# Performance work log

Measured on AMD Instinct MI355X. Metric: run time of the kernel, lower is better.

Reference implementation:

```python
import jax, jax.numpy as jnp
import numpy as np

HEAD_DIM = 128
N_HEADS = 32
DIM = 4096
SEQ = 2048
BSZ = 2


def apply_rotary(x, cos, sin):
    # x: [b, s, h, d]; cos/sin: [s, d//2]
    xr = x.reshape(*x.shape[:-1], -1, 2)  # [b, s, h, d/2, 2]
    xe, xo = xr[..., 0], xr[..., 1]
    c = cos[None, :, None, :]
    s = sin[None, :, None, :]
    oe = xe * c - xo * s
    oo = xe * s + xo * c
    return jnp.stack([oe, oo], axis=-1).reshape(x.shape)


def setup_inputs() -> dict:
    key = jax.random.key(0)
    ks = jax.random.split(key, 8)
    x = jax.random.normal(ks[0], (BSZ, SEQ, DIM), dtype=jnp.float32)
    scale = 1.0 / np.sqrt(DIM)
    wq = jax.random.normal(ks[1], (DIM, DIM), dtype=jnp.float32) * scale
    wk = jax.random.normal(ks[2], (DIM, DIM), dtype=jnp.float32) * scale
    wv = jax.random.normal(ks[3], (DIM, DIM), dtype=jnp.float32) * scale
    wo = jax.random.normal(ks[4], (DIM, DIM), dtype=jnp.float32) * scale
    # RoPE frequencies (LLaMA convention)
    inv_freq = 1.0 / (10000.0 ** (np.arange(0, HEAD_DIM, 2, dtype=np.float32) / HEAD_DIM))
    t = np.arange(SEQ, dtype=np.float32)
    angles = np.outer(t, inv_freq)  # [S, d/2]
    freqs_cos = jnp.asarray(np.cos(angles))
    freqs_sin = jnp.asarray(np.sin(angles))
    # additive causal mask
    mask = jnp.where(jnp.triu(jnp.ones((SEQ, SEQ), dtype=bool), k=1), -jnp.inf, 0.0)
    mask = mask.astype(jnp.float32)[None, None, :, :]
    return {"x": x, "wq": wq, "wk": wk, "wv": wv, "wo": wo,
            "freqs_cos": freqs_cos, "freqs_sin": freqs_sin, "mask": mask,
            "start_pos": 0}


def reference(x, wq, wk, wv, wo, freqs_cos, freqs_sin, mask, start_pos):
    bsz, seqlen, _ = x.shape
    xq = (x @ wq.T).reshape(bsz, seqlen, N_HEADS, HEAD_DIM)
    xk = (x @ wk.T).reshape(bsz, seqlen, N_HEADS, HEAD_DIM)
    xv = (x @ wv.T).reshape(bsz, seqlen, N_HEADS, HEAD_DIM)
    xq = apply_rotary(xq, freqs_cos, freqs_sin)
    xk = apply_rotary(xk, freqs_cos, freqs_sin)
    # [b, h, s, d]
    q = xq.transpose(0, 2, 1, 3)
    k = xk.transpose(0, 2, 1, 3)
    v = xv.transpose(0, 2, 1, 3)
    scores = jnp.einsum("bhqd,bhkd->bhqk", q, k) / np.sqrt(HEAD_DIM)
    scores = scores + mask
    probs = jax.nn.softmax(scores.astype(jnp.float32), axis=-1).astype(q.dtype)
    out = jnp.einsum("bhqk,bhkd->bhqd", probs, v)
    out = out.transpose(0, 2, 1, 3).reshape(bsz, seqlen, -1)
    return out @ wo.T
```

## Files before the change

### kernel.cpp

```cpp
#include <hip/hip_runtime.h>
#include <stdint.h>

#define DIMK 4096
#define HD 128
#define NH 32
#define SEQL 2048
#define BSZN 2
#define NROWS (BSZN*SEQL)

typedef __bf16 bf16x8 __attribute__((ext_vector_type(8)));
typedef float f32x4 __attribute__((ext_vector_type(4)));
typedef unsigned short u16;
typedef unsigned int u32;

__device__ __forceinline__ float bf2f(u16 h){
  u32 u = ((u32)h) << 16; float f;
  __builtin_memcpy(&f, &u, 4); return f;
}
__device__ __forceinline__ u16 f2bf(float f){
  u32 u; __builtin_memcpy(&u, &f, 4);
  return (u16)((u + 0x7fffu + ((u >> 16) & 1u)) >> 16);
}

__device__ __forceinline__ void gld_lds16(const void* g, void* l){
  __builtin_amdgcn_global_load_lds(
      (__attribute__((address_space(1))) void*)(uintptr_t)g,
      (__attribute__((address_space(3))) void*)(uintptr_t)l, 16, 0, 0);
}

#define BARX __builtin_amdgcn_s_barrier()
#define LGKM0 asm volatile("s_waitcnt lgkmcnt(0)" ::: "memory")
#define VMC6  asm volatile("s_waitcnt vmcnt(6)"  ::: "memory")
#define SP1 __builtin_amdgcn_s_setprio(1)
#define SP0 __builtin_amdgcn_s_setprio(0)

#define LDA4(MB, Ab) do{ \
  _Pragma("unroll") for (int mi = 0; mi < 4; ++mi){ \
    const int m_ = (MB) + mi; \
    const short* _p = (Ab) + (m_>>2)*8192 + (m_&3)*2048 + rdA; \
    aF[mi][0] = *(const bf16x8*)(_p + ch0); \
    aF[mi][1] = *(const bf16x8*)(_p + ch1); } }while(0)

#define LDB2(NB, Bb) do{ \
  _Pragma("unroll") for (int ni = 0; ni < 2; ++ni){ \
    const int n_ = (NB) + ni; \
    const short* _p = (Bb) + (n_>>1)*8192 + (n_&1)*4096 + rdB; \
    bF[ni][0] = *(const bf16x8*)(_p + ch0); \
    bF[ni][1] = *(const bf16x8*)(_p + ch1); } }while(0)

#define MFMA16(MB, NB) do{ \
  _Pragma("unroll") for (int ks = 0; ks < 2; ++ks) \
  _Pragma("unroll") for (int mi = 0; mi < 4; ++mi) \
  _Pragma("unroll") for (int ni = 0; ni < 2; ++ni) \
    acc[(MB)+mi][(NB)+ni] = __builtin_amdgcn_mfma_f32_16x16x32_bf16( \
        aF[mi][ks], bF[ni][ks], acc[(MB)+mi][(NB)+ni], 0, 0, 0); }while(0)

#define STG_A(buf,h,kt) do{ \
    size_t _o = ((size_t)(h)<<19) + (size_t)(kt)*64; \
    short* _d = dA + (buf)*32768 + (h)*8192; \
    gld_lds16(sA[0]+_o, _d); gld_lds16(sA[1]+_o, _d+512); }while(0)

#define STG_B(buf,h,kt) do{ \
    size_t _o = ((size_t)(h)<<19) + (size_t)(kt)*64; \
    short* _d = dB + (buf)*32768 + (h)*8192; \
    gld_lds16(sB[0]+_o, _d); gld_lds16(sB[1]+_o, _d+512); }while(0)

template<int OUTF32>
__device__ __forceinline__ void gemm256_core(const u16* __restrict__ A,
                                             const u16* __restrict__ B,
                                             void* __restrict__ Cv,
                                             short* SMEM)
{
  const int tid  = threadIdx.x;
  const int wave = tid >> 6, lane = tid & 63;
  const int wm = wave >> 2, wn = wave & 3;
  const int g = lane >> 4, c16 = lane & 15;

  const int bid = blockIdx.x;
  const int xcd = bid & 7, cc = bid >> 3;
  const int bx = (xcd & 3)*4 + (cc & 3);
  const int by = (xcd >> 2)*8 + (cc >> 2);
  const int m0 = bx*256, n0 = by*256;

  const int ch0 = ((g ^ (c16 & 7)) << 3);
  const int ch1 = ch0 ^ 32;
  const int rdA = wm*1024 + c16*64;
  const int rdB = wn*1024 + c16*64;

  const int swzc = (((lane & 7) ^ ((lane >> 3) & 7)) << 3);
  const u16* sA[2]; const u16* sB[2];
  #pragma unroll
  for (int p = 0; p < 2; ++p){
    int rr = wave*16 + p*8 + (lane >> 3);
    sA[p] = A + (size_t)(m0 + rr)*DIMK + swzc;
    sB[p] = B + (size_t)(n0 + rr)*DIMK + swzc;
  }
  short* const dA = SMEM + wave*1024;
  short* const dB = SMEM + 16384 + wave*1024;

  const short* A0 = SMEM;
  const short* B0 = SMEM + 16384;
  const short* A1 = SMEM + 32768;
  const short* B1 = SMEM + 49152;

  f32x4 acc[8][4];
  #pragma unroll
  for (int m = 0; m < 8; ++m)
    #pragma unroll
    for (int n = 0; n < 4; ++n)
      acc[m][n] = (f32x4){0.f, 0.f, 0.f, 0.f};

  bf16x8 aF[4][2], bF[2][2];

  STG_A(0,0,0); STG_B(0,1,0); STG_A(0,1,0); STG_B(0,0,0);
  STG_A(1,0,1); STG_B(1,1,1); STG_A(1,1,1);
  VMC6; BARX;

  #pragma unroll 1
  for (int i = 0; i < 32; ++i){
    const int t1 = (2*i+1) & 63, t2 = (2*i+2) & 63, t3 = (2*i+3) & 63;
    LDA4(0, A0); LDB2(0, B0);
    STG_B(1, 0, t1);
    BARX; LGKM0;
    SP1; MFMA16(0, 0); SP0;
    BARX;
    LDB2(2, B0);
    STG_A(0, 0, t2);
    BARX; LGKM0;
    SP1; MFMA16(0, 2); SP0;
    BARX;
    LDA4(4, A0);
    STG_B(0, 1, t2);
    BARX; LGKM0;
    SP1; MFMA16(4, 2); SP0;
    BARX;
    LDB2(0, B0);
    STG_A(0, 1, t2);
    VMC6;
    BARX; LGKM0;
    SP1; MFMA16(4, 0); SP0;
    BARX;
    LDA4(0, A1); LDB2(0, B1);
    STG_B(0, 0, t2);
    BARX; LGKM0;
    SP1; MFMA16(0, 0); SP0;
    BARX;
    LDB2(2, B1);
    STG_A(1, 0, t3);
    BARX; LGKM0;
    SP1; MFMA16(0, 2); SP0;
    BARX;
    LDA4(4, A1);
    STG_B(1, 1, t3);
    BARX; LGKM0;
    SP1; MFMA16(4, 2); SP0;
    BARX;
    LDB2(0, B1);
    STG_A(1, 1, t3);
    VMC6;
    BARX; LGKM0;
    SP1; MFMA16(4, 0); SP0;
    BARX;
  }

  if constexpr (OUTF32 == 0){
    u16* C = (u16*)Cv;
    #pragma unroll
    for (int m = 0; m < 8; ++m){
      int row0 = m0 + (m*2 + wm)*16 + g*4;
      #pragma unroll
      for (int n = 0; n < 4; ++n){
        int col = n0 + (n*4 + wn)*16 + c16;
        #pragma unroll
        for (int r = 0; r < 4; ++r)
          C[(size_t)(row0 + r)*DIMK + col] = f2bf(acc[m][n][r]);
      }
    }
  } else {
    float* C = (float*)Cv;
    #pragma unroll
    for (int m = 0; m < 8; ++m){
      int row0 = m0 + (m*2 + wm)*16 + g*4;
      #pragma unroll
      for (int n = 0; n < 4; ++n){
        int col = n0 + (n*4 + wn)*16 + c16;
        #pragma unroll
        for (int r = 0; r < 4; ++r)
          C[(size_t)(row0 + r)*DIMK + col] = acc[m][n][r];
      }
    }
  }
}

__global__ __launch_bounds__(512, 2) void gemm_bf16_kernel(const u16* __restrict__ A,
    const u16* __restrict__ B, u16* __restrict__ C)
{
  __shared__ __align__(16) short SMEM[65536];
  gemm256_core<0>(A, B, C, SMEM);
}

__global__ __launch_bounds__(512, 2) void gemm_f32_kernel(const u16* __restrict__ A,
    const u16* __restrict__ B, float* __restrict__ C)
{
  __shared__ __align__(16) short SMEM[65536];
  gemm256_core<1>(A, B, C, SMEM);
}

__global__ __launch_bounds__(256) void cvt_kernel(const float* __restrict__ src,
                                                  u16* __restrict__ dst, int n8)
{
  int t = blockIdx.x*256 + threadIdx.x;
  if (t >= n8) return;
  const f32x4* s = (const f32x4*)src + (size_t)t*2;
  f32x4 a = s[0], b = s[1];
  ushort4 lo, hi;
  lo.x = f2bf(a[0]); lo.y = f2bf(a[1]); lo.z = f2bf(a[2]); lo.w = f2bf(a[3]);
  hi.x = f2bf(b[0]); hi.y = f2bf(b[1]); hi.z = f2bf(b[2]); hi.w = f2bf(b[3]);
  ushort4* d = (ushort4*)dst + (size_t)t*2;
  d[0] = lo; d[1] = hi;
}

__global__ __launch_bounds__(256) void transpose_kernel(const u16* __restrict__ v,
                                                        u16* __restrict__ vt)
{
  __shared__ u16 tile[64][72];
  const int t  = threadIdx.x;
  const int s0 = blockIdx.x * 64;
  const int d0 = blockIdx.y * 64;
  const int bh = blockIdx.z;
  const int b = bh >> 5, h = bh & 31;

  #pragma unroll
  for (int i = 0; i < 4; ++i){
    int row = i*16 + (t >> 4);
    int cc  = (t & 15) * 4;
    uint2 val = *(const uint2*)(v + (size_t)(b*SEQL + s0 + row)*DIMK + h*HD + d0 + cc);
    const u16* p4 = (const u16*)&val;
    #pragma unroll
    for (int j = 0; j < 4; ++j) tile[cc + j][row] = p4[j];
  }
  __syncthreads();
  #pragma unroll
  for (int i = 0; i < 4; ++i){
    int drow = i*16 + (t >> 4);
    int sc   = (t & 15) * 4;
    uint2 o; u16* po = (u16*)&o;
    #pragma unroll
    for (int j = 0; j < 4; ++j) po[j] = tile[drow][sc + j];
    *(uint2*)(vt + ((size_t)(b*NH + h)*HD + d0 + drow)*SEQL + s0 + sc) = o;
  }
}

__global__ __launch_bounds__(256) void rope_kernel(const u16* __restrict__ qsrc,
    const u16* __restrict__ ksrc, u16* __restrict__ qdst, u16* __restrict__ kdst,
    const float* __restrict__ fc, const float* __restrict__ fs)
{
  const size_t PER = (size_t)NROWS * DIMK / 8;
  size_t t = (size_t)blockIdx.x * 256 + threadIdx.x;
  const u16* src = qsrc; u16* dst = qdst;
  if (t >= PER){ src = ksrc; dst = kdst; t -= PER; }
  size_t e0 = t * 8;
  int row = (int)(e0 >> 12);
  int col = (int)(e0 & (DIMK-1));
  int s  = row & (SEQL-1);
  int i0 = (col & (HD-1)) >> 1;

  uint4 raw = *(const uint4*)(src + e0);
  u16* xs = (u16*)&raw;
  f32x4 c4 = *(const f32x4*)(fc + s*64 + i0);
  f32x4 s4 = *(const f32x4*)(fs + s*64 + i0);
  #pragma unroll
  for (int j = 0; j < 4; ++j){
    float e = bf2f(xs[2*j]), o = bf2f(xs[2*j+1]);
    float c = c4[j], sn = s4[j];
    xs[2*j]   = f2bf(e*c - o*sn);
    xs[2*j+1] = f2bf(e*sn + o*c);
  }
  *(uint4*)(dst + e0) = raw;
}

__device__ __forceinline__ void stage_k_tile(const u16* kb, int s0, short* Ksd,
                                             int wave, int g, int c16){
  #pragma unroll
  for (int it = 0; it < 4; ++it){
    int rbase = it*16 + wave*4;
    int row = rbase + g;
    gld_lds16(kb + (size_t)(s0 + row)*DIMK + ((c16 ^ (row & 7)) << 3),
              Ksd + rbase*128);
  }
}
__device__ __forceinline__ void stage_v_tile(const u16* vb, int s0, short* Vd,
                                             int wave, int lane){
  const int sc = lane & 7, rg = lane >> 3;
  #pragma unroll
  for (int it = 0; it < 4; ++it){
    int rbase = (it*4 + wave)*8;
    int row = rbase + rg;
    gld_lds16(vb + (size_t)row*SEQL + s0 + ((sc ^ (row & 7)) << 3),
              Vd + rbase*64);
  }
}

__global__ __launch_bounds__(256) void flash_kernel(const u16* __restrict__ Q,
    const u16* __restrict__ K, const u16* __restrict__ Vt, u16* __restrict__ AO)
{
  __shared__ short Ks[64*128];
  __shared__ short Vs[2*128*64];
  __shared__ short Ps[4*32*64];

  const int bh = blockIdx.x;
  const int qt = 15 - (int)blockIdx.y;
  const int b = bh >> 5, h = bh & 31;
  const int tid = threadIdx.x;
  const int wave = tid >> 6, lane = tid & 63;
  const int g = lane >> 4, c16 = lane & 15;
  const int qr0 = qt*128 + wave*32;

  const u16* kb = K  + (size_t)(b*SEQL)*DIMK + h*HD;
  const u16* vb = Vt + (size_t)(b*NH + h)*HD*SEQL;
  short* Pw = Ps + wave*(32*64);

  stage_k_tile(kb, 0, Ks, wave, g, c16);
  stage_v_tile(vb, 0, Vs, wave, lane);

  bf16x8 qa[2][4];
  #pragma unroll
  for (int rt = 0; rt < 2; ++rt){
    const u16* qp = Q + (size_t)(b*SEQL + qr0 + rt*16 + c16)*DIMK + h*HD + g*8;
    #pragma unroll
    for (int kc = 0; kc < 4; ++kc)
      qa[rt][kc] = *(const bf16x8*)(qp + kc*32);
  }

  f32x4 oacc[2][8];
  #pragma unroll
  for (int rt = 0; rt < 2; ++rt)
    #pragma unroll
    for (int dt = 0; dt < 8; ++dt)
      oacc[rt][dt] = (f32x4){0.f, 0.f, 0.f, 0.f};
  float m_st[2][4], l_st[2][4];
  #pragma unroll
  for (int rt = 0; rt < 2; ++rt)
    #pragma unroll
    for (int r = 0; r < 4; ++r){ m_st[rt][r] = -1e30f; l_st[rt][r] = 0.f; }

  const int nsteps = 2*(qt + 1);
  for (int kt = 0; kt < nsteps; ++kt){
    const int s0 = kt*64;
    const short* Vsc = Vs + (kt & 1)*(128*64);
    const bool alive = (s0 <= qr0 + 31);

    __syncthreads();

    f32x4 sacc[2][4];
    if (alive){
      #pragma unroll
      for (int rt = 0; rt < 2; ++rt)
        #pragma unroll
        for (int ct = 0; ct < 4; ++ct)
          sacc[rt][ct] = (f32x4){0.f, 0.f, 0.f, 0.f};
      __builtin_amdgcn_s_setprio(1);
      #pragma unroll
      for (int kc = 0; kc < 4; ++kc){
        #pragma unroll
        for (int ct = 0; ct < 4; ++ct){
          int row = ct*16 + c16;
          bf16x8 bfr = *(const bf16x8*)(Ks + row*128 + (((g + 4*kc) ^ (row & 7)) << 3));
          sacc[0][ct] = __builtin_amdgcn_mfma_f32_16x16x32_bf16(qa[0][kc], bfr, sacc[0][ct], 0, 0, 0);
          sacc[1][ct] = __builtin_amdgcn_mfma_f32_16x16x32_bf16(qa[1][kc], bfr, sacc[1][ct], 0, 0, 0);
        }
      }
      __builtin_amdgcn_s_setprio(0);
    }

    __syncthreads();

    if (kt + 1 < nsteps){
      stage_k_tile(kb, s0 + 64, Ks, wave, g, c16);
      stage_v_tile(vb, s0 + 64, Vs + ((kt+1) & 1)*(128*64), wave, lane);
    }

    if (alive){
      const float scale = 0.08838834764831845f;
      #pragma unroll
      for (int rt = 0; rt < 2; ++rt){
        int rowb = qr0 + rt*16 + g*4;
        #pragma unroll
        for (int ct = 0; ct < 4; ++ct){
          int scol = s0 + ct*16 + c16;
          #pragma unroll
          for (int r = 0; r < 4; ++r){
            float v = sacc[rt][ct][r] * scale;
            sacc[rt][ct][r] = (scol <= rowb + r) ? v : -1e30f;
          }
        }
      }

      #pragma unroll
      for (int rt = 0; rt < 2; ++rt){
        #pragma unroll
        for (int r = 0; r < 4; ++r){
          float mx = fmaxf(fmaxf(sacc[rt][0][r], sacc[rt][1][r]),
                           fmaxf(sacc[rt][2][r], sacc[rt][3][r]));
          #pragma unroll
          for (int off = 1; off < 16; off <<= 1)
            mx = fmaxf(mx, __shfl_xor(mx, off));
          float mn = fmaxf(m_st[rt][r], mx);
          float al = __expf(m_st[rt][r] - mn);
          m_st[rt][r] = mn;
          float sum = 0.f;
          #pragma unroll
          for (int ct = 0; ct < 4; ++ct){
            float pv = __expf(sacc[rt][ct][r] - mn);
            sacc[rt][ct][r] = pv;
            sum += pv;
          }
          #pragma unroll
          for (int off = 1; off < 16; off <<= 1)
            sum += __shfl_xor(sum, off);
          l_st[rt][r] = l_st[rt][r]*al + sum;
          #pragma unroll
          for (int dt = 0; dt < 8; ++dt)
            oacc[rt][dt][r] *= al;
        }
      }

      #pragma unroll
      for (int rt = 0; rt < 2; ++rt)
        #pragma unroll
        for (int ct = 0; ct < 4; ++ct)
          #pragma unroll
          for (int r = 0; r < 4; ++r){
            int prow = rt*16 + g*4 + r;
            int pcol = ct*16 + c16;
            Pw[prow*64 + ((((pcol >> 3) ^ (prow & 7)) << 3) | (pcol & 7))] =
                (short)f2bf(sacc[rt][ct][r]);
          }

      asm volatile("s_waitcnt lgkmcnt(0)" ::: "memory");
      __builtin_amdgcn_sched_barrier(0);

      __builtin_amdgcn_s_setprio(1);
      #pragma unroll
      for (int kc2 = 0; kc2 < 2; ++kc2){
        int pr0 = c16, pr1 = 16 + c16;
        bf16x8 pf0 = *(const bf16x8*)(Pw + pr0*64 + (((g + 4*kc2) ^ (pr0 & 7)) << 3));
        bf16x8 pf1 = *(const bf16x8*)(Pw + pr1*64 + (((g + 4*kc2) ^ (pr1 & 7)) << 3));
        #pragma unroll
        for (int dt = 0; dt < 8; ++dt){
          int vr = dt*16 + c16;
          bf16x8 vf = *(const bf16x8*)(Vsc + vr*64 + (((g + 4*kc2) ^ (vr & 7)) << 3));
          oacc[0][dt] = __builtin_amdgcn_mfma_f32_16x16x32_bf16(pf0, vf, oacc[0][dt], 0, 0, 0);
          oacc[1][dt] = __builtin_amdgcn_mfma_f32_16x16x32_bf16(pf1, vf, oacc[1][dt], 0, 0, 0);
        }
      }
      __builtin_amdgcn_s_setprio(0);
    }
  }

  #pragma unroll
  for (int rt = 0; rt < 2; ++rt){
    float inv[4];
    #pragma unroll
    for (int r = 0; r < 4; ++r) inv[r] = 1.0f / l_st[rt][r];
    #pragma unroll
    for (int dt = 0; dt < 8; ++dt){
      #pragma unroll
      for (int r = 0; r < 4; ++r){
        int qrow = qr0 + rt*16 + g*4 + r;
        int col  = h*HD + dt*16 + c16;
        AO[(size_t)(b*SEQL + qrow)*DIMK + col] = f2bf(oacc[rt][dt][r] * inv[r]);
      }
    }
  }
}

extern "C" void kernel_launch(void* const* d_in, const int* in_sizes, int n_in,
                              void* d_out, int out_size, void* d_ws, size_t ws_size,
                              hipStream_t stream)
{
  const float* x  = (const float*)d_in[0];
  const float* wq = (const float*)d_in[1];
  const float* wk = (const float*)d_in[2];
  const float* wv = (const float*)d_in[3];
  const float* wo = (const float*)d_in[4];
  const float* fc = (const float*)d_in[5];
  const float* fs = (const float*)d_in[6];
  float* out = (float*)d_out;

  const size_t TEN  = (size_t)NROWS * DIMK;
  const size_t TENB = TEN * sizeof(u16);
  const int N8 = (int)(TEN / 8);

  const dim3 GG(256), B512(512), B256(256);
  const dim3 FG(64, 16);

  if (ws_size >= 8 * TENB){
    u16* xb   = (u16*)d_ws;
    u16* wb   = xb   + TEN;
    u16* qb   = wb   + TEN;
    u16* kb   = qb   + TEN;
    u16* vraw = kb   + TEN;
    u16* vtb  = vraw + TEN;
    u16* qro  = vtb  + TEN;
    u16* kro  = qro  + TEN;
    cvt_kernel<<<dim3(8192), B256, 0, stream>>>(x,  xb, N8);
    cvt_kernel<<<dim3(8192), B256, 0, stream>>>(wq, wb, N8);
    gemm_bf16_kernel<<<GG, B512, 0, stream>>>(xb, wb, qb);
    cvt_kernel<<<dim3(8192), B256, 0, stream>>>(wk, wb, N8);
    gemm_bf16_kernel<<<GG, B512, 0, stream>>>(xb, wb, kb);
    cvt_kernel<<<dim3(8192), B256, 0, stream>>>(wv, wb, N8);
    gemm_bf16_kernel<<<GG, B512, 0, stream>>>(xb, wb, vraw);
    transpose_kernel<<<dim3(32, 2, 64), B256, 0, stream>>>(vraw, vtb);
    rope_kernel<<<dim3(16384), B256, 0, stream>>>(qb, kb, qro, kro, fc, fs);
    flash_kernel<<<FG, B256, 0, stream>>>(qro, kro, vtb, vraw);
    cvt_kernel<<<dim3(8192), B256, 0, stream>>>(wo, xb, N8);
    gemm_f32_kernel<<<GG, B512, 0, stream>>>(vraw, xb, out);
  } else if (ws_size >= 4 * TENB){
    u16* xb  = (u16*)d_out;
    u16* wb  = xb + TEN;
    u16* qb  = (u16*)d_ws;
    u16* kb  = qb + TEN;
    u16* vtb = kb + TEN;
    u16* s3  = vtb + TEN;
    cvt_kernel<<<dim3(8192), B256, 0, stream>>>(x,  xb, N8);
    cvt_kernel<<<dim3(8192), B256, 0, stream>>>(wq, wb, N8);
    gemm_bf16_kernel<<<GG, B512, 0, stream>>>(xb, wb, qb);
    cvt_kernel<<<dim3(8192), B256, 0, stream>>>(wk, wb, N8);
    gemm_bf16_kernel<<<GG, B512, 0, stream>>>(xb, wb, kb);
    cvt_kernel<<<dim3(8192), B256, 0, stream>>>(wv, wb, N8);
    gemm_bf16_kernel<<<GG, B512, 0, stream>>>(xb, wb, s3);
    transpose_kernel<<<dim3(32, 2, 64), B256, 0, stream>>>(s3, vtb);
    rope_kernel<<<dim3(16384), B256, 0, stream>>>(qb, kb, s3, xb, fc, fs);
    flash_kernel<<<FG, B256, 0, stream>>>(s3, xb, vtb, qb);
    cvt_kernel<<<dim3(8192), B256, 0, stream>>>(wo, kb, N8);
    gemm_f32_kernel<<<GG, B512, 0, stream>>>(qb, kb, out);
  }
}
```

Baseline: 1.037 ms.

## Widen flash KV tile to 128, remap GEMM block order, add partial LDS waits

The flash kernel now processes 128-key tiles per step instead of 64, halving loop iterations and barriers. K and V each use a single 128x128 LDS buffer, and V is restaged only after the PV pass. This removes double buffering for V and adds an extra __syncthreads per step, so load latency may be exposed. Causally masked 16-column chunks are skipped per wave. Separately, the GEMM block-to-tile mapping is changed to a new XCD swizzle, and an lgkmcnt(8) wait is inserted before some barriers.

```diff
diff --git a/kernel.cpp b/kernel.cpp
--- a/kernel.cpp
+++ b/kernel.cpp
@@ -30,6 +30,7 @@
 
 #define BARX __builtin_amdgcn_s_barrier()
 #define LGKM0 asm volatile("s_waitcnt lgkmcnt(0)" ::: "memory")
+#define LGKM8 asm volatile("s_waitcnt lgkmcnt(8)" ::: "memory")
 #define VMC6  asm volatile("s_waitcnt vmcnt(6)"  ::: "memory")
 #define SP1 __builtin_amdgcn_s_setprio(1)
 #define SP0 __builtin_amdgcn_s_setprio(0)
@@ -77,9 +78,8 @@
   const int g = lane >> 4, c16 = lane & 15;
 
   const int bid = blockIdx.x;
-  const int xcd = bid & 7, cc = bid >> 3;
-  const int bx = (xcd & 3)*4 + (cc & 3);
-  const int by = (xcd >> 2)*8 + (cc >> 2);
+  const int wg  = (bid & 7) * 32 + (bid >> 3);
+  const int bx = wg >> 4, by = wg & 15;
   const int m0 = bx*256, n0 = by*256;
 
   const int ch0 = ((g ^ (c16 & 7)) << 3);
@@ -121,6 +121,7 @@
     const int t1 = (2*i+1) & 63, t2 = (2*i+2) & 63, t3 = (2*i+3) & 63;
     LDA4(0, A0); LDB2(0, B0);
     STG_B(1, 0, t1);
+    LGKM8;
     BARX; LGKM0;
     SP1; MFMA16(0, 0); SP0;
     BARX;
@@ -142,6 +143,7 @@
     BARX;
     LDA4(0, A1); LDB2(0, B1);
     STG_B(0, 0, t2);
+    LGKM8;
     BARX; LGKM0;
     SP1; MFMA16(0, 0); SP0;
     BARX;
@@ -279,33 +281,33 @@
   *(uint4*)(dst + e0) = raw;
 }
 
-__device__ __forceinline__ void stage_k_tile(const u16* kb, int s0, short* Ksd,
-                                             int wave, int g, int c16){
-  #pragma unroll
-  for (int it = 0; it < 4; ++it){
+__device__ __forceinline__ void stage_k128(const u16* kb, int s0, short* Ksd,
+                                           int wave, int g, int c16){
+  #pragma unroll
+  for (int it = 0; it < 8; ++it){
     int rbase = it*16 + wave*4;
     int row = rbase + g;
     gld_lds16(kb + (size_t)(s0 + row)*DIMK + ((c16 ^ (row & 7)) << 3),
               Ksd + rbase*128);
   }
 }
-__device__ __forceinline__ void stage_v_tile(const u16* vb, int s0, short* Vd,
-                                             int wave, int lane){
-  const int sc = lane & 7, rg = lane >> 3;
-  #pragma unroll
-  for (int it = 0; it < 4; ++it){
-    int rbase = (it*4 + wave)*8;
+__device__ __forceinline__ void stage_v128(const u16* vb, int s0, short* Vd,
+                                           int wave, int lane){
+  const int sc = lane & 15, rg = lane >> 4;
+  #pragma unroll
+  for (int it = 0; it < 8; ++it){
+    int rbase = it*16 + wave*4;
     int row = rbase + rg;
     gld_lds16(vb + (size_t)row*SEQL + s0 + ((sc ^ (row & 7)) << 3),
-              Vd + rbase*64);
+              Vd + rbase*128);
   }
 }
 
 __global__ __launch_bounds__(256) void flash_kernel(const u16* __restrict__ Q,
     const u16* __restrict__ K, const u16* __restrict__ Vt, u16* __restrict__ AO)
 {
-  __shared__ short Ks[64*128];
-  __shared__ short Vs[2*128*64];
+  __shared__ short Ks[128*128];
+  __shared__ short Vs[128*128];
   __shared__ short Ps[4*32*64];
 
   const int bh = blockIdx.x;
@@ -315,13 +317,14 @@
   const int wave = tid >> 6, lane = tid & 63;
   const int g = lane >> 4, c16 = lane & 15;
   const int qr0 = qt*128 + wave*32;
+  const int rmax = qr0 + 31;
 
   const u16* kb = K  + (size_t)(b*SEQL)*DIMK + h*HD;
   const u16* vb = Vt + (size_t)(b*NH + h)*HD*SEQL;
   short* Pw = Ps + wave*(32*64);
 
-  stage_k_tile(kb, 0, Ks, wave, g, c16);
-  stage_v_tile(vb, 0, Vs, wave, lane);
+  stage_k128(kb, 0, Ks, wave, g, c16);
+  stage_v128(vb, 0, Vs, wave, lane);
 
   bf16x8 qa[2][4];
   #pragma unroll
@@ -344,86 +347,85 @@
     #pragma unroll
     for (int r = 0; r < 4; ++r){ m_st[rt][r] = -1e30f; l_st[rt][r] = 0.f; }
 
-  const int nsteps = 2*(qt + 1);
+  const int nsteps = qt + 1;
   for (int kt = 0; kt < nsteps; ++kt){
-    const int s0 = kt*64;
-    const short* Vsc = Vs + (kt & 1)*(128*64);
-    const bool alive = (s0 <= qr0 + 31);
+    const int s0 = kt*128;
 
     __syncthreads();
 
-    f32x4 sacc[2][4];
-    if (alive){
-      #pragma unroll
-      for (int rt = 0; rt < 2; ++rt)
-        #pragma unroll
-        for (int ct = 0; ct < 4; ++ct)
-          sacc[rt][ct] = (f32x4){0.f, 0.f, 0.f, 0.f};
-      __builtin_amdgcn_s_setprio(1);
-      #pragma unroll
-      for (int kc = 0; kc < 4; ++kc){
-        #pragma unroll
-        for (int ct = 0; ct < 4; ++ct){
-          int row = ct*16 + c16;
-          bf16x8 bfr = *(const bf16x8*)(Ks + row*128 + (((g + 4*kc) ^ (row & 7)) << 3));
-          sacc[0][ct] = __builtin_amdgcn_mfma_f32_16x16x32_bf16(qa[0][kc], bfr, sacc[0][ct], 0, 0, 0);
-          sacc[1][ct] = __builtin_amdgcn_mfma_f32_16x16x32_bf16(qa[1][kc], bfr, sacc[1][ct], 0, 0, 0);
+    f32x4 sacc[2][8];
+    #pragma unroll
+    for (int rt = 0; rt < 2; ++rt)
+      #pragma unroll
+      for (int ct = 0; ct < 8; ++ct)
+        sacc[rt][ct] = (f32x4){0.f, 0.f, 0.f, 0.f};
+    __builtin_amdgcn_s_setprio(1);
+    #pragma unroll
+    for (int kc = 0; kc < 4; ++kc){
+      #pragma unroll
+      for (int ct = 0; ct < 8; ++ct){
+        if (s0 + ct*16 > rmax) continue;
+        int row = ct*16 + c16;
+        bf16x8 bfr = *(const bf16x8*)(Ks + row*128 + (((g + 4*kc) ^ (row & 7)) << 3));
+        sacc[0][ct] = __builtin_amdgcn_mfma_f32_16x16x32_bf16(qa[0][kc], bfr, sacc[0][ct], 0, 0, 0);
+        sacc[1][ct] = __builtin_amdgcn_mfma_f32_16x16x32_bf16(qa[1][kc], bfr, sacc[1][ct], 0, 0, 0);
+      }
+    }
+    __builtin_amdgcn_s_setprio(0);
+
+    __syncthreads();
+
+    if (kt + 1 < nsteps)
+      stage_k128(kb, s0 + 128, Ks, wave, g, c16);
+
+    const float scale = 0.08838834764831845f;
+    #pragma unroll
+    for (int rt = 0; rt < 2; ++rt){
+      int rowb = qr0 + rt*16 + g*4;
+      #pragma unroll
+      for (int ct = 0; ct < 8; ++ct){
+        int scol = s0 + ct*16 + c16;
+        #pragma unroll
+        for (int r = 0; r < 4; ++r){
+          float v = sacc[rt][ct][r] * scale;
+          sacc[rt][ct][r] = (scol <= rowb + r) ? v : -1e30f;
         }
       }
-      __builtin_amdgcn_s_setprio(0);
-    }
-
-    __syncthreads();
-
-    if (kt + 1 < nsteps){
-      stage_k_tile(kb, s0 + 64, Ks, wave, g, c16);
-      stage_v_tile(vb, s0 + 64, Vs + ((kt+1) & 1)*(128*64), wave, lane);
-    }
-
-    if (alive){
-      const float scale = 0.08838834764831845f;
-      #pragma unroll
-      for (int rt = 0; rt < 2; ++rt){
-        int rowb = qr0 + rt*16 + g*4;
-        #pragma unroll
-        for (int ct = 0; ct < 4; ++ct){
-          int scol = s0 + ct*16 + c16;
-          #pragma unroll
-          for (int r = 0; r < 4; ++r){
-            float v = sacc[rt][ct][r] * scale;
-            sacc[rt][ct][r] = (scol <= rowb + r) ? v : -1e30f;
-          }
+    }
+
+    #pragma unroll
+    for (int rt = 0; rt < 2; ++rt){
+      #pragma unroll
+      for (int r = 0; r < 4; ++r){
+        float mx = sacc[rt][0][r];
+        #pragma unroll
+        for (int ct = 1; ct < 8; ++ct) mx = fmaxf(mx, sacc[rt][ct][r]);
+        #pragma unroll
+        for (int off = 1; off < 16; off <<= 1)
+          mx = fmaxf(mx, __shfl_xor(mx, off));
+        float mn = fmaxf(m_st[rt][r], mx);
+        float al = __expf(m_st[rt][r] - mn);
+        m_st[rt][r] = mn;
+        float sum = 0.f;
+        #pragma unroll
+        for (int ct = 0; ct < 8; ++ct){
+          float pv = __expf(sacc[rt][ct][r] - mn);
+          sacc[rt][ct][r] = pv;
+          sum += pv;
         }
-      }
-
-      #pragma unroll
-      for (int rt = 0; rt < 2; ++rt){
-        #pragma unroll
-        for (int r = 0; r < 4; ++r){
-          float mx = fmaxf(fmaxf(sacc[rt][0][r], sacc[rt][1][r]),
-                           fmaxf(sacc[rt][2][r], sacc[rt][3][r]));
-          #pragma unroll
-          for (int off = 1; off < 16; off <<= 1)
-            mx = fmaxf(mx, __shfl_xor(mx, off));
-          float mn = fmaxf(m_st[rt][r], mx);
-          float al = __expf(m_st[rt][r] - mn);
-          m_st[rt][r] = mn;
-          float sum = 0.f;
-          #pragma unroll
-          for (int ct = 0; ct < 4; ++ct){
-            float pv = __expf(sacc[rt][ct][r] - mn);
-            sacc[rt][ct][r] = pv;
-            sum += pv;
-          }
-          #pragma unroll
-          for (int off = 1; off < 16; off <<= 1)
-            sum += __shfl_xor(sum, off);
-          l_st[rt][r] = l_st[rt][r]*al + sum;
-          #pragma unroll
-          for (int dt = 0; dt < 8; ++dt)
-            oacc[rt][dt][r] *= al;
-        }
-      }
+        #pragma unroll
+        for (int off = 1; off < 16; off <<= 1)
+          sum += __shfl_xor(sum, off);
+        l_st[rt][r] = l_st[rt][r]*al + sum;
+        #pragma unroll
+        for (int dt = 0; dt < 8; ++dt)
+          oacc[rt][dt][r] *= al;
+      }
+    }
+
+    #pragma unroll
+    for (int c = 0; c < 2; ++c){
+      if (s0 + c*64 > rmax) continue;
 
       #pragma unroll
       for (int rt = 0; rt < 2; ++rt)
@@ -434,7 +436,7 @@
             int prow = rt*16 + g*4 + r;
             int pcol = ct*16 + c16;
             Pw[prow*64 + ((((pcol >> 3) ^ (prow & 7)) << 3) | (pcol & 7))] =
-                (short)f2bf(sacc[rt][ct][r]);
+                (short)f2bf(sacc[rt][c*4 + ct][r]);
           }
 
       asm volatile("s_waitcnt lgkmcnt(0)" ::: "memory");
@@ -449,13 +451,19 @@
         #pragma unroll
         for (int dt = 0; dt < 8; ++dt){
           int vr = dt*16 + c16;
-          bf16x8 vf = *(const bf16x8*)(Vsc + vr*64 + (((g + 4*kc2) ^ (vr & 7)) << 3));
+          int chv = c*8 + kc2*4 + g;
+          bf16x8 vf = *(const bf16x8*)(Vs + vr*128 + ((chv ^ (vr & 7)) << 3));
           oacc[0][dt] = __builtin_amdgcn_mfma_f32_16x16x32_bf16(pf0, vf, oacc[0][dt], 0, 0, 0);
           oacc[1][dt] = __builtin_amdgcn_mfma_f32_16x16x32_bf16(pf1, vf, oacc[1][dt], 0, 0, 0);
         }
       }
       __builtin_amdgcn_s_setprio(0);
     }
+
+    __syncthreads();
+
+    if (kt + 1 < nsteps)
+      stage_v128(vb, s0 + 128, Vs, wave, lane);
   }
 
   #pragma unroll
```

Measured after the change: 1.013 ms. 1.02x faster.
